# Optimization experiments

Measured on AMD Instinct MI355X. Metric: run time of the kernel, lower is better.

Reference implementation:

```python
import jax, jax.numpy as jnp
import numpy as np

NB, NA, NC, NH, NW = 128, 5, 80, 28, 28
NT = 50
ANCHORS = jnp.array([2.8, 4.8, 5.1, 10.2, 6.4, 16.3, 9.2, 19.8, 14.1, 23.7], dtype=jnp.float32)
ANCHOR_W = ANCHORS[0::2]  # [NA]
ANCHOR_H = ANCHORS[1::2]
OBJECT_SCALE = 5.0
NOOBJECT_SCALE = 1.0
CLASS_SCALE = 1.0
COORD_SCALE = 1.0
SIL_THRESH = 0.6


def iou_cxcywh(b1, b2):
    # center-format IoU, matches bbox_ious(x1y1x2y2=False); inputs broadcastable (...,4)
    x1, y1, w1, h1 = b1[..., 0], b1[..., 1], b1[..., 2], b1[..., 3]
    x2, y2, w2, h2 = b2[..., 0], b2[..., 1], b2[..., 2], b2[..., 3]
    mx = jnp.minimum(x1 - w1 / 2, x2 - w2 / 2)
    Mx = jnp.maximum(x1 + w1 / 2, x2 + w2 / 2)
    my = jnp.minimum(y1 - h1 / 2, y2 - h2 / 2)
    My = jnp.maximum(y1 + h1 / 2, y2 + h2 / 2)
    cw = w1 + w2 - (Mx - mx)
    ch = h1 + h2 - (My - my)
    inter = jnp.where((cw > 0) & (ch > 0), cw * ch, 0.0)
    union = w1 * h1 + w2 * h2 - inter
    return inter / union


def build_targets(pred_boxes, target):
    # pred_boxes: [NB, NA, NH, NW, 4] grid-unit cxcywh (already detached)
    tgt = target.reshape(NB, NT, 5)
    gcls = tgt[..., 0]
    gx = tgt[..., 1] * NW
    gy = tgt[..., 2] * NH
    gw = tgt[..., 3] * NW
    gh = tgt[..., 4] * NH
    gt_boxes = jnp.stack([gx, gy, gw, gh], -1)  # [NB, NT, 4]

    # silence mask: any-GT IoU > thresh -> conf_mask 0, else noobject_scale
    pb = pred_boxes.reshape(NB, NA * NH * NW, 4)
    ious = iou_cxcywh(pb[:, :, None, :], gt_boxes[:, None, :, :])  # [NB, nAnchors, NT]
    max_iou = jnp.max(ious, axis=2)
    conf_mask0 = jnp.where(max_iou > SIL_THRESH, 0.0, NOOBJECT_SCALE).reshape(NB, NA, NH, NW)

    # best anchor per GT by wh-only IoU at origin
    z_na = jnp.zeros((NA,), jnp.float32)
    anc = jnp.stack([z_na, z_na, ANCHOR_W, ANCHOR_H], -1)  # [NA,4]
    zg = jnp.zeros_like(gw)
    gt_wh = jnp.stack([zg, zg, gw, gh], -1)  # [NB,NT,4]
    a_iou = iou_cxcywh(gt_wh[:, :, None, :], anc[None, None, :, :])  # [NB,NT,NA]
    best_n = jnp.argmax(a_iou, axis=2)  # [NB,NT] (first max, matches strict > loop)

    gi = jnp.floor(gx).astype(jnp.int32)
    gj = jnp.floor(gy).astype(jnp.int32)
    flat_idx = ((jnp.arange(NB)[:, None] * NA + best_n) * NH + gj) * NW + gi  # [NB,NT]

    assigned_pred = pred_boxes.reshape(NB * NA * NH * NW, 4)[flat_idx]  # [NB,NT,4]
    iou_gt_pred = iou_cxcywh(gt_boxes, assigned_pred)  # [NB,NT]
    aw = ANCHOR_W[best_n]
    ah = ANCHOR_H[best_n]

    idx = flat_idx.reshape(-1)
    grid0 = jnp.zeros((NB * NA * NH * NW,), jnp.float32)

    def sc(init_flat, v):
        return init_flat.at[idx].set(v.reshape(-1)).reshape(NB, NA, NH, NW)

    ones = jnp.ones((NB, NT), jnp.float32)
    coord_mask = sc(grid0, ones)
    cls_mask = sc(grid0, ones)
    conf_mask = sc(conf_mask0.reshape(-1), jnp.full((NB, NT), OBJECT_SCALE, jnp.float32))
    tx = sc(grid0, gx - gi.astype(jnp.float32))
    ty = sc(grid0, gy - gj.astype(jnp.float32))
    tw = sc(grid0, jnp.log(gw / aw))
    th = sc(grid0, jnp.log(gh / ah))
    tconf = sc(grid0, iou_gt_pred)
    tcls = sc(grid0, gcls)
    return coord_mask, conf_mask, cls_mask, tx, ty, tw, th, tconf, tcls


def _smooth_l1_sum(a, b):
    d = a - b
    ad = jnp.abs(d)
    return jnp.sum(jnp.where(ad < 1.0, 0.5 * d * d, ad - 0.5))


def _forward(output, target):
    out = output.reshape(NB, NA, 5 + NC, NH, NW)
    x = jax.nn.sigmoid(out[:, :, 0])
    y = jax.nn.sigmoid(out[:, :, 1])
    w = out[:, :, 2]
    h = out[:, :, 3]
    conf = jax.nn.sigmoid(out[:, :, 4])
    cls_logits = jnp.transpose(out[:, :, 5:], (0, 1, 3, 4, 2))  # [NB,NA,NH,NW,NC]

    gx = jnp.arange(NW, dtype=jnp.float32)[None, None, None, :]
    gy = jnp.arange(NH, dtype=jnp.float32)[None, None, :, None]
    sg = jax.lax.stop_gradient
    px = sg(x) + gx
    py = sg(y) + gy
    pw = jnp.exp(sg(w)) * ANCHOR_W[None, :, None, None]
    ph = jnp.exp(sg(h)) * ANCHOR_H[None, :, None, None]
    pred_boxes = jnp.stack([px, py, pw, ph], -1)  # [NB,NA,NH,NW,4]

    bt = jax.lax.stop_gradient(build_targets(pred_boxes, target))
    coord_mask, conf_mask, cls_mask, tx, ty, tw, th, tconf, tcls = bt
    conf_mask = jnp.sqrt(conf_mask)

    loss_x = COORD_SCALE * _smooth_l1_sum(x * coord_mask, tx * coord_mask) / 2.0
    loss_y = COORD_SCALE * _smooth_l1_sum(y * coord_mask, ty * coord_mask) / 2.0
    loss_w = COORD_SCALE * _smooth_l1_sum(w * coord_mask, tw * coord_mask) / 2.0
    loss_h = COORD_SCALE * _smooth_l1_sum(h * coord_mask, th * coord_mask) / 2.0
    loss_conf = jnp.sum((conf * conf_mask - tconf * conf_mask) ** 2) / 2.0

    # focal loss (gamma=2, alpha=1, sum reduction) over cells with cls_mask==1
    logp = jax.nn.log_softmax(cls_logits, axis=-1)
    logp_t = jnp.take_along_axis(logp, tcls[..., None].astype(jnp.int32), axis=-1)[..., 0]
    p_t = jnp.exp(logp_t)
    focal = -((1.0 - p_t) ** 2) * logp_t
    loss_cls = CLASS_SCALE * jnp.sum(cls_mask * focal)

    return loss_x + loss_y + loss_w + loss_h + loss_conf + loss_cls


def setup_inputs() -> dict:
    key = jax.random.key(0)
    k1, k2, k3 = jax.random.split(key, 3)
    output = jax.random.normal(k1, (NB, NA * (5 + NC), NH, NW), dtype=jnp.float32)
    u = jax.random.uniform(k2, (NB, NT, 4), dtype=jnp.float32)
    xy = 0.1 + 0.8 * u[..., :2]   # x in (0.1,0.9) -> never 0, no early break
    wh = 0.05 + 0.45 * u[..., 2:]
    cls_id = jax.random.randint(k3, (NB, NT, 1), 0, NC).astype(jnp.float32)
    target = jnp.concatenate([cls_id, xy, wh], axis=-1).reshape(NB, NT * 5)
    return {"output": output, "target": target}


def reference(output, target):
    return _forward(output, target)
```

## Files before the change

### kernel.cpp

```cpp
#include <hip/hip_runtime.h>
#include <math.h>

#define NBB 128
#define NAA 5
#define NCC 80
#define NHH 28
#define NWW 28
#define NTT 50
#define CH  85
#define HW  784
#define CELLS 3920
#define NREC  6400

__constant__ float c_AW[5] = {2.8f, 5.1f, 6.4f, 9.2f, 14.1f};
__constant__ float c_AH[5] = {4.8f, 10.2f, 16.3f, 19.8f, 23.7f};

__device__ __forceinline__ float sigmoidf_(float x) {
    return 1.0f / (1.0f + __expf(-x));
}

__device__ __forceinline__ float smooth_l1(float d) {
    float ad = fabsf(d);
    return (ad < 1.0f) ? 0.5f * d * d : ad - 0.5f;
}

__global__ __launch_bounds__(256) void prep_conf_loss(
    const float* __restrict__ out, const float* __restrict__ tgt,
    int* __restrict__ recIdx, float* __restrict__ recF,
    float* __restrict__ d_out)
{
    __shared__ float L2[NTT], R2[NTT], T2[NTT], B2[NTT], AR[NTT];
    __shared__ int   rCell[NTT];
    __shared__ float rTc[NTT];
    __shared__ float red[256];

    const int b   = blockIdx.y;
    const int tid = threadIdx.x;

    float tx = 0.f, ty = 0.f, tw = 0.f, th = 0.f, tcls = 0.f;

    if (tid < NTT) {
        const float* tp = tgt + b * NTT * 5 + tid * 5;
        float cls = tp[0];
        float gx = tp[1] * NWW;
        float gy = tp[2] * NHH;
        float gw = tp[3] * NWW;
        float gh = tp[4] * NHH;
        float ga = gw * gh;

        L2[tid] = gx - gw * 0.5f;
        R2[tid] = gx + gw * 0.5f;
        T2[tid] = gy - gh * 0.5f;
        B2[tid] = gy + gh * 0.5f;
        AR[tid] = ga;

        int best = 0; float bestI = -1.0f;
        #pragma unroll
        for (int a = 0; a < 5; ++a) {
            float inter = fminf(gw, c_AW[a]) * fminf(gh, c_AH[a]);
            float uni   = ga + c_AW[a] * c_AH[a] - inter;
            float iou   = inter / uni;
            if (iou > bestI) { bestI = iou; best = a; }
        }
        int gi = (int)floorf(gx);
        int gj = (int)floorf(gy);
        int cell = (best * NHH + gj) * NWW + gi;

        const float* op = out + ((size_t)(b * NAA + best) * CH) * HW + gj * NWW + gi;
        float px = sigmoidf_(op[0])      + (float)gi;
        float py = sigmoidf_(op[HW])     + (float)gj;
        float pw = __expf(op[2 * HW]) * c_AW[best];
        float ph = __expf(op[3 * HW]) * c_AH[best];

        float mx = fminf(px - pw * 0.5f, gx - gw * 0.5f);
        float Mx = fmaxf(px + pw * 0.5f, gx + gw * 0.5f);
        float my = fminf(py - ph * 0.5f, gy - gh * 0.5f);
        float My = fmaxf(py + ph * 0.5f, gy + gh * 0.5f);
        float cw  = pw + gw - (Mx - mx);
        float chh = ph + gh - (My - my);
        float inter = (cw > 0.f && chh > 0.f) ? cw * chh : 0.f;
        float uni   = pw * ph + ga - inter;

        rCell[tid] = cell;
        rTc[tid]   = inter / uni;

        tx = gx - (float)gi;
        ty = gy - (float)gj;
        tw = __logf(gw / c_AW[best]);
        th = __logf(gh / c_AH[best]);
        tcls = cls;
    }
    __syncthreads();

    if (blockIdx.x == 0 && tid < NTT) {
        int cell = rCell[tid];
        bool active = true;
        for (int t2 = tid + 1; t2 < NTT; ++t2)
            if (rCell[t2] == cell) active = false;
        int r = b * NTT + tid;
        recIdx[r]          = active ? cell : -1;
        recF[0 * NREC + r] = tx;
        recF[1 * NREC + r] = ty;
        recF[2 * NREC + r] = tw;
        recF[3 * NREC + r] = th;
        recF[4 * NREC + r] = tcls;
    }

    const int cell = blockIdx.x * 256 + tid;
    float term = 0.0f;

    if (cell < CELLS) {
        int a  = cell / HW;
        int hw = cell - a * HW;
        int wi = hw % NWW;
        int hj = hw / NWW;
        const float* op = out + ((size_t)(b * NAA + a) * CH) * HW + hw;

        float px   = sigmoidf_(op[0])  + (float)wi;
        float py   = sigmoidf_(op[HW]) + (float)hj;
        float pw   = __expf(op[2 * HW]) * c_AW[a];
        float ph   = __expf(op[3 * HW]) * c_AH[a];
        float conf = sigmoidf_(op[4 * HW]);

        float l1 = px - pw * 0.5f, r1 = px + pw * 0.5f;
        float t1 = py - ph * 0.5f, b1 = py + ph * 0.5f;
        float a1 = pw * ph;

        bool flag = false;
        #pragma unroll 5
        for (int j = 0; j < NTT; ++j) {
            float cw  = fminf(r1, R2[j]) - fmaxf(l1, L2[j]);
            float chh = fminf(b1, B2[j]) - fmaxf(t1, T2[j]);
            float inter = (cw > 0.f && chh > 0.f) ? cw * chh : 0.f;
            flag = flag || (inter * 1.6f > 0.6f * (a1 + AR[j]));
        }

        bool assigned = false; float tc = 0.f;
        for (int j = 0; j < NTT; ++j) {
            if (rCell[j] == cell) { assigned = true; tc = rTc[j]; }
        }

        if (assigned) { float d = conf - tc; term = 2.5f * d * d; }
        else if (!flag) { term = 0.5f * conf * conf; }
    }

    red[tid] = term;
    __syncthreads();
    for (int s = 128; s > 0; s >>= 1) {
        if (tid < s) red[tid] += red[tid + s];
        __syncthreads();
    }
    if (tid == 0) atomicAdd(d_out, red[0]);
}

__global__ __launch_bounds__(256) void assigned_loss(
    const float* __restrict__ out, const int* __restrict__ recIdx,
    const float* __restrict__ recF, float* __restrict__ d_out)
{
    const int wave = threadIdx.x >> 6;
    const int lane = threadIdx.x & 63;
    const int r    = blockIdx.x * 4 + wave;

    __shared__ float ws[4];
    float contrib = 0.0f;

    int cell = recIdx[r];
    if (cell >= 0) {
        int b  = r / NTT;
        int a  = cell / HW;
        int hw = cell - a * HW;
        const float* op = out + ((size_t)(b * NAA + a) * CH) * HW + hw;

        float l0 = op[(5 + lane) * HW];
        float l1 = (lane < 16) ? op[(5 + 64 + lane) * HW] : -INFINITY;

        float m = fmaxf(l0, l1);
        for (int o = 32; o >= 1; o >>= 1) m = fmaxf(m, __shfl_xor(m, o));
        float s = __expf(l0 - m) + ((lane < 16) ? __expf(l1 - m) : 0.0f);
        for (int o = 32; o >= 1; o >>= 1) s += __shfl_xor(s, o);

        int t = (int)recF[4 * NREC + r];
        float lt = (t < 64) ? __shfl(l0, t) : __shfl(l1, t - 64);
        float logpt = lt - m - __logf(s);
        float pt = __expf(logpt);
        float focal = -(1.0f - pt) * (1.0f - pt) * logpt;

        if (lane == 0) {
            float tx = recF[0 * NREC + r];
            float ty = recF[1 * NREC + r];
            float tw = recF[2 * NREC + r];
            float th = recF[3 * NREC + r];
            float x = sigmoidf_(op[0]);
            float y = sigmoidf_(op[HW]);
            float w = op[2 * HW];
            float h = op[3 * HW];
            contrib = focal +
                      0.5f * (smooth_l1(x - tx) + smooth_l1(y - ty) +
                              smooth_l1(w - tw) + smooth_l1(h - th));
        }
    }

    if (lane == 0) ws[wave] = contrib;
    __syncthreads();
    if (threadIdx.x == 0)
        atomicAdd(d_out, ws[0] + ws[1] + ws[2] + ws[3]);
}

extern "C" void kernel_launch(void* const* d_in, const int* in_sizes, int n_in,
                              void* d_out, int out_size, void* d_ws, size_t ws_size,
                              hipStream_t stream) {
    const float* out_p = (const float*)d_in[0];
    const float* tgt_p = (const float*)d_in[1];
    float* loss = (float*)d_out;

    int*   recIdx = (int*)d_ws;
    float* recF   = (float*)d_ws + NREC;

    hipMemsetAsync(loss, 0, (size_t)out_size * sizeof(float), stream);

    prep_conf_loss<<<dim3(16, NBB), dim3(256), 0, stream>>>(
        out_p, tgt_p, recIdx, recF, loss);
    assigned_loss<<<dim3(NREC / 4), dim3(256), 0, stream>>>(
        out_p, recIdx, recF, loss);
}
```

Measured before the change: 267.5 us.

## Fuse assigned-cell class/coord loss into the conf-loss kernel

```diff
diff --git a/kernel.cpp b/kernel.cpp
--- a/kernel.cpp
+++ b/kernel.cpp
@@ -10,7 +10,6 @@
 #define CH  85
 #define HW  784
 #define CELLS 3920
-#define NREC  6400
 
 __constant__ float c_AW[5] = {2.8f, 5.1f, 6.4f, 9.2f, 14.1f};
 __constant__ float c_AH[5] = {4.8f, 10.2f, 16.3f, 19.8f, 23.7f};
@@ -24,20 +23,20 @@
     return (ad < 1.0f) ? 0.5f * d * d : ad - 0.5f;
 }
 
-__global__ __launch_bounds__(256) void prep_conf_loss(
+__global__ __launch_bounds__(256) void region_loss_fused(
     const float* __restrict__ out, const float* __restrict__ tgt,
-    int* __restrict__ recIdx, float* __restrict__ recF,
     float* __restrict__ d_out)
 {
     __shared__ float L2[NTT], R2[NTT], T2[NTT], B2[NTT], AR[NTT];
     __shared__ int   rCell[NTT];
-    __shared__ float rTc[NTT];
+    __shared__ float rTc[NTT], rTx[NTT], rTy[NTT], rTw[NTT], rTh[NTT];
+    __shared__ int   rCls[NTT];
+    __shared__ unsigned char rActive[NTT];
     __shared__ float red[256];
+    __shared__ float waveS[4];
 
     const int b   = blockIdx.y;
     const int tid = threadIdx.x;
-
-    float tx = 0.f, ty = 0.f, tw = 0.f, th = 0.f, tcls = 0.f;
 
     if (tid < NTT) {
         const float* tp = tgt + b * NTT * 5 + tid * 5;
@@ -83,27 +82,20 @@
 
         rCell[tid] = cell;
         rTc[tid]   = inter / uni;
-
-        tx = gx - (float)gi;
-        ty = gy - (float)gj;
-        tw = __logf(gw / c_AW[best]);
-        th = __logf(gh / c_AH[best]);
-        tcls = cls;
+        rTx[tid]   = gx - (float)gi;
+        rTy[tid]   = gy - (float)gj;
+        rTw[tid]   = __logf(gw / c_AW[best]);
+        rTh[tid]   = __logf(gh / c_AH[best]);
+        rCls[tid]  = (int)cls;
     }
     __syncthreads();
 
-    if (blockIdx.x == 0 && tid < NTT) {
+    if (tid < NTT) {
         int cell = rCell[tid];
-        bool active = true;
+        unsigned char active = 1;
         for (int t2 = tid + 1; t2 < NTT; ++t2)
-            if (rCell[t2] == cell) active = false;
-        int r = b * NTT + tid;
-        recIdx[r]          = active ? cell : -1;
-        recF[0 * NREC + r] = tx;
-        recF[1 * NREC + r] = ty;
-        recF[2 * NREC + r] = tw;
-        recF[3 * NREC + r] = th;
-        recF[4 * NREC + r] = tcls;
+            if (rCell[t2] == cell) active = 0;
+        rActive[tid] = active;
     }
 
     const int cell = blockIdx.x * 256 + tid;
@@ -144,31 +136,17 @@
         else if (!flag) { term = 0.5f * conf * conf; }
     }
 
-    red[tid] = term;
-    __syncthreads();
-    for (int s = 128; s > 0; s >>= 1) {
-        if (tid < s) red[tid] += red[tid + s];
-        __syncthreads();
-    }
-    if (tid == 0) atomicAdd(d_out, red[0]);
-}
-
-__global__ __launch_bounds__(256) void assigned_loss(
-    const float* __restrict__ out, const int* __restrict__ recIdx,
-    const float* __restrict__ recF, float* __restrict__ d_out)
-{
-    const int wave = threadIdx.x >> 6;
-    const int lane = threadIdx.x & 63;
-    const int r    = blockIdx.x * 4 + wave;
-
-    __shared__ float ws[4];
+    const int wave = tid >> 6;
+    const int lane = tid & 63;
+    const int j    = blockIdx.x * 4 + wave;
     float contrib = 0.0f;
 
-    int cell = recIdx[r];
-    if (cell >= 0) {
-        int b  = r / NTT;
-        int a  = cell / HW;
-        int hw = cell - a * HW;
+    __syncthreads();
+
+    if (j < NTT && rActive[j]) {
+        int rc = rCell[j];
+        int a  = rc / HW;
+        int hw = rc - a * HW;
         const float* op = out + ((size_t)(b * NAA + a) * CH) * HW + hw;
 
         float l0 = op[(5 + lane) * HW];
@@ -179,31 +157,32 @@
         float s = __expf(l0 - m) + ((lane < 16) ? __expf(l1 - m) : 0.0f);
         for (int o = 32; o >= 1; o >>= 1) s += __shfl_xor(s, o);
 
-        int t = (int)recF[4 * NREC + r];
+        int t = rCls[j];
         float lt = (t < 64) ? __shfl(l0, t) : __shfl(l1, t - 64);
         float logpt = lt - m - __logf(s);
         float pt = __expf(logpt);
         float focal = -(1.0f - pt) * (1.0f - pt) * logpt;
 
         if (lane == 0) {
-            float tx = recF[0 * NREC + r];
-            float ty = recF[1 * NREC + r];
-            float tw = recF[2 * NREC + r];
-            float th = recF[3 * NREC + r];
             float x = sigmoidf_(op[0]);
             float y = sigmoidf_(op[HW]);
             float w = op[2 * HW];
             float h = op[3 * HW];
             contrib = focal +
-                      0.5f * (smooth_l1(x - tx) + smooth_l1(y - ty) +
-                              smooth_l1(w - tw) + smooth_l1(h - th));
+                      0.5f * (smooth_l1(x - rTx[j]) + smooth_l1(y - rTy[j]) +
+                              smooth_l1(w - rTw[j]) + smooth_l1(h - rTh[j]));
         }
     }
+    if (lane == 0) waveS[wave] = contrib;
 
-    if (lane == 0) ws[wave] = contrib;
+    red[tid] = term;
     __syncthreads();
-    if (threadIdx.x == 0)
-        atomicAdd(d_out, ws[0] + ws[1] + ws[2] + ws[3]);
+    for (int s = 128; s > 0; s >>= 1) {
+        if (tid < s) red[tid] += red[tid + s];
+        __syncthreads();
+    }
+    if (tid == 0)
+        atomicAdd(d_out, red[0] + waveS[0] + waveS[1] + waveS[2] + waveS[3]);
 }
 
 extern "C" void kernel_launch(void* const* d_in, const int* in_sizes, int n_in,
@@ -213,13 +192,8 @@
     const float* tgt_p = (const float*)d_in[1];
     float* loss = (float*)d_out;
 
-    int*   recIdx = (int*)d_ws;
-    float* recF   = (float*)d_ws + NREC;
-
     hipMemsetAsync(loss, 0, (size_t)out_size * sizeof(float), stream);
 
-    prep_conf_loss<<<dim3(16, NBB), dim3(256), 0, stream>>>(
-        out_p, tgt_p, recIdx, recF, loss);
-    assigned_loss<<<dim3(NREC / 4), dim3(256), 0, stream>>>(
-        out_p, recIdx, recF, loss);
+    region_loss_fused<<<dim3(16, NBB), dim3(256), 0, stream>>>(
+        out_p, tgt_p, loss);
 }
```

New measurement: 235.3 us. -12.1%, faster.
